# Kernel optimization log

Measured on AMD Instinct MI355X. Metric: run time of the kernel, lower is better.

Reference implementation:

```python
import jax, jax.numpy as jnp
import numpy as np
import math

B, S, D = 16, 2048, 128

def setup_inputs() -> dict:
    key = jax.random.key(0)
    k1, k2, k3, k4 = jax.random.split(key, 4)
    query = jax.random.normal(k1, (B, S, D), dtype=jnp.float32)
    key_t = jax.random.normal(k2, (B, S, D), dtype=jnp.float32)
    value = jax.random.normal(k3, (B, S, D), dtype=jnp.float32)
    attn_mask = jax.random.randint(k4, (B, S, S), 0, 2).astype(bool)
    return {"query": query, "key": key_t, "value": value, "attn_mask": attn_mask}

def reference(query, key, value, attn_mask):
    # score = Q K^T / sqrt(d)  -> [B, Sq, Sk]
    scale = 1.0 / math.sqrt(query.shape[-1])
    score = jnp.einsum('bqd,bkd->bqk', query, key) * scale
    # faithful quirk: masked positions are replaced by the VALUE 1e-9 (not -inf)
    mask_score = jnp.where(attn_mask, jnp.float32(1e-9), score)
    # faithful quirk: softmax over dim=1 (the query axis), as in the torch source
    score_matrix = jax.nn.softmax(mask_score, axis=1)
    # output = softmax(scores) @ V  -> [B, Sq, D]
    output = jnp.einsum('bqk,bkd->bqd', score_matrix, value)
    return output
```

## Files before the change

### kernel.cpp

```cpp
#include <hip/hip_runtime.h>
#include <math.h>

#define NB 16
#define SS 2048
#define DQ 128
#define SCALE 0.08838834764831845f

typedef __bf16 bf16x8 __attribute__((ext_vector_type(8)));
typedef unsigned short ushort8_t __attribute__((ext_vector_type(8)));
typedef float floatx4 __attribute__((ext_vector_type(4)));

__device__ __forceinline__ unsigned short f2bf(float x) {
  unsigned int u = __float_as_uint(x);
  u += 0x7fffu + ((u >> 16) & 1u);
  return (unsigned short)(u >> 16);
}
union FragU { ushort8_t u; bf16x8 b; };
__device__ __forceinline__ bf16x8 ld_frag(const unsigned short* p) {
  FragU t; t.u = *(const ushort8_t*)p; return t.b;
}
__device__ __forceinline__ floatx4 mfma16(bf16x8 a, bf16x8 b, floatx4 c) {
  return __builtin_amdgcn_mfma_f32_16x16x32_bf16(a, b, c, 0, 0, 0);
}

__device__ __forceinline__ void bar_lds() {
  asm volatile("s_waitcnt lgkmcnt(0)\n\ts_barrier" ::: "memory");
}


__global__ void zero_accum(float* __restrict__ O) {
  float* p = O + (size_t)blockIdx.x * SS * DQ + 16 * DQ;
#pragma unroll
  for (int i = 0; i < 8; ++i) p[threadIdx.x + 256 * i] = 0.f;
}

__global__ __launch_bounds__(256, 4) void pass1_colsum(
    const float* __restrict__ Q, const float* __restrict__ K,
    const int* __restrict__ M, float* __restrict__ O)
{
  const int k0  = blockIdx.x * 64;
  const int b   = blockIdx.y;
  const int qc  = blockIdx.z;
  const int tid = threadIdx.x;
  const int w = tid >> 6, lane = tid & 63, l15 = lane & 15, quad = lane >> 4;

  __shared__ unsigned short Kbf[64][136];
  __shared__ unsigned short Qbf[64][136];
  __shared__ float red[4][64];

  const float* Qb = Q + (size_t)b * SS * DQ;
  const float* Kb = K + (size_t)b * SS * DQ;
  const int*   Mb = M + (size_t)b * SS * SS;

  const int srow = tid >> 5;
  const int sc4  = (tid & 31) * 4;

#pragma unroll
  for (int r = 0; r < 8; ++r) {
    int row = srow + r * 8;
    float4 v = *(const float4*)(Kb + (size_t)(k0 + row) * DQ + sc4);
    *(ushort4*)&Kbf[row][sc4] = make_ushort4(f2bf(v.x), f2bf(v.y), f2bf(v.z), f2bf(v.w));
  }

  const int qlane = 16 * w + l15;

  float4 qreg[8];
  int4 mv_nxt[4];
  {
    const int q0 = qc * 512;
#pragma unroll
    for (int r = 0; r < 8; ++r)
      qreg[r] = *(const float4*)(Qb + (size_t)(q0 + srow + r * 8) * DQ + sc4);
#pragma unroll
    for (int i = 0; i < 4; ++i)
      mv_nxt[i] = *(const int4*)(Mb + (size_t)(q0 + qlane) * SS + k0 + 16 * i + quad * 4);
  }

  float colacc[16];
#pragma unroll
  for (int t = 0; t < 16; ++t) colacc[t] = 0.f;

  for (int qi = 0; qi < 8; ++qi) {
    bar_lds();
    int4 mv[4] = {mv_nxt[0], mv_nxt[1], mv_nxt[2], mv_nxt[3]};
#pragma unroll
    for (int r = 0; r < 8; ++r) {
      float4 v = qreg[r];
      *(ushort4*)&Qbf[srow + r * 8][sc4] =
          make_ushort4(f2bf(v.x), f2bf(v.y), f2bf(v.z), f2bf(v.w));
    }
    bar_lds();
    if (qi < 7) {
      const int qn = qc * 512 + (qi + 1) * 64;
#pragma unroll
      for (int r = 0; r < 8; ++r)
        qreg[r] = *(const float4*)(Qb + (size_t)(qn + srow + r * 8) * DQ + sc4);
#pragma unroll
      for (int i = 0; i < 4; ++i)
        mv_nxt[i] = *(const int4*)(Mb + (size_t)(qn + qlane) * SS + k0 + 16 * i + quad * 4);
    }

    floatx4 acc[4];
#pragma unroll
    for (int i = 0; i < 4; ++i) acc[i] = (floatx4){0.f, 0.f, 0.f, 0.f};
#pragma unroll
    for (int d0 = 0; d0 < DQ; d0 += 32) {
      bf16x8 bq = ld_frag(&Qbf[qlane][d0 + quad * 8]);
#pragma unroll
      for (int i = 0; i < 4; ++i) {
        bf16x8 ak = ld_frag(&Kbf[16 * i + l15][d0 + quad * 8]);
        acc[i] = mfma16(ak, bq, acc[i]);
      }
    }
#pragma unroll
    for (int i = 0; i < 4; ++i) {
      int mm[4] = {mv[i].x, mv[i].y, mv[i].z, mv[i].w};
#pragma unroll
      for (int r = 0; r < 4; ++r) {
        float s = mm[r] ? 1e-9f : acc[i][r] * SCALE;
        colacc[i * 4 + r] += __expf(s);
      }
    }
  }

#pragma unroll
  for (int t = 0; t < 16; ++t) {
    colacc[t] += __shfl_xor(colacc[t], 1, 64);
    colacc[t] += __shfl_xor(colacc[t], 2, 64);
    colacc[t] += __shfl_xor(colacc[t], 4, 64);
    colacc[t] += __shfl_xor(colacc[t], 8, 64);
  }
  if (l15 == 0) {
#pragma unroll
    for (int i = 0; i < 4; ++i)
#pragma unroll
      for (int r = 0; r < 4; ++r)
        red[w][16 * i + quad * 4 + r] = colacc[i * 4 + r];
  }
  bar_lds();
  if (tid < 64) {
    float s = red[0][tid] + red[1][tid] + red[2][tid] + red[3][tid];
    atomicAdd(O + (size_t)b * SS * DQ + 16 * DQ + k0 + tid, s);
  }
}

__global__ void combine_linv(float* __restrict__ O) {
  const int b  = blockIdx.x;
  const int jb = blockIdx.y * 4;
  float* Ob = O + (size_t)b * SS * DQ;
#pragma unroll
  for (int it = 0; it < 8; ++it) {
    int k = threadIdx.x + 256 * it;
    float inv = 1.0f / Ob[16 * DQ + k];
#pragma unroll
    for (int j = 0; j < 4; ++j)
      Ob[(size_t)(64 * (jb + j)) * DQ + k] = inv;
  }
}

__global__ __launch_bounds__(256, 2) void pass2_out(
    const float* __restrict__ Q, const float* __restrict__ K,
    const float* __restrict__ V, const int* __restrict__ M,
    float* __restrict__ O)
{
  const int b = blockIdx.y, q0 = blockIdx.x * 64;
  const int tid = threadIdx.x;
  const int w = tid >> 6, lane = tid & 63, l15 = lane & 15, quad = lane >> 4;

  __shared__ unsigned short Kbf[64][136];
  __shared__ unsigned short Es[64][72];
  __shared__ unsigned short Wt[128][72];
  __shared__ float Li[SS];

  const float* Qb = Q + (size_t)b * SS * DQ;
  const float* Kb = K + (size_t)b * SS * DQ;
  const float* Vb = V + (size_t)b * SS * DQ;
  const int*   Mb = M + (size_t)b * SS * SS;

  const int srow = tid >> 5;
  const int sc4  = (tid & 31) * 4;

  {
    const float* src = O + ((size_t)b * SS + q0) * DQ;
#pragma unroll
    for (int r = 0; r < 2; ++r) {
      int idx = (tid + r * 256) * 4;
      *(float4*)&Li[idx] = *(const float4*)(src + idx);
    }
  }
  FragU qf[4];
  {
    const float* qrow = Qb + (size_t)(q0 + 16 * w + l15) * DQ;
#pragma unroll
    for (int i = 0; i < 4; ++i) {
      float4 a = *(const float4*)(qrow + 32 * i + quad * 8);
      float4 c = *(const float4*)(qrow + 32 * i + quad * 8 + 4);
      qf[i].u = (ushort8_t){f2bf(a.x), f2bf(a.y), f2bf(a.z), f2bf(a.w),
                            f2bf(c.x), f2bf(c.y), f2bf(c.z), f2bf(c.w)};
    }
  }

  floatx4 accO[8];
#pragma unroll
  for (int j = 0; j < 8; ++j) accO[j] = (floatx4){0.f, 0.f, 0.f, 0.f};

  const int* mrow = Mb + (size_t)(q0 + 16 * w + l15) * SS;

  float4 kreg[8], vreg[8];
  int4 mv_nxt[4];
  const int vk2 = (tid >> 5) * 2;
  {
#pragma unroll
    for (int r = 0; r < 8; ++r)
      kreg[r] = *(const float4*)(Kb + (size_t)(srow + r * 8) * DQ + sc4);
#pragma unroll
    for (int r = 0; r < 4; ++r) {
      int k2 = vk2 + r * 16;
      vreg[2 * r]     = *(const float4*)(Vb + (size_t)(k2)     * DQ + sc4);
      vreg[2 * r + 1] = *(const float4*)(Vb + (size_t)(k2 + 1) * DQ + sc4);
    }
#pragma unroll
    for (int j = 0; j < 4; ++j)
      mv_nxt[j] = *(const int4*)(mrow + 16 * j + quad * 4);
  }

  for (int k0 = 0; k0 < SS; k0 += 64) {
    bar_lds();
    int4 mv[4] = {mv_nxt[0], mv_nxt[1], mv_nxt[2], mv_nxt[3]};

#pragma unroll
    for (int r = 0; r < 8; ++r) {
      float4 v = kreg[r];
      *(ushort4*)&Kbf[srow + r * 8][sc4] =
          make_ushort4(f2bf(v.x), f2bf(v.y), f2bf(v.z), f2bf(v.w));
    }
#pragma unroll
    for (int r = 0; r < 4; ++r) {
      int k2 = vk2 + r * 16;
      float fa[4] = {vreg[2*r].x, vreg[2*r].y, vreg[2*r].z, vreg[2*r].w};
      float fb[4] = {vreg[2*r+1].x, vreg[2*r+1].y, vreg[2*r+1].z, vreg[2*r+1].w};
#pragma unroll
      for (int i = 0; i < 4; ++i) {
        int d  = sc4 + i;
        int kk = k2 ^ ((((unsigned)d >> 2) & 7) << 3);
        *(ushort2*)&Wt[d][kk] = make_ushort2(f2bf(fa[i]), f2bf(fb[i]));
      }
    }
    bar_lds();

    if (k0 + 64 < SS) {
      const int kn = k0 + 64;
#pragma unroll
      for (int r = 0; r < 8; ++r)
        kreg[r] = *(const float4*)(Kb + (size_t)(kn + srow + r * 8) * DQ + sc4);
#pragma unroll
      for (int r = 0; r < 4; ++r) {
        int k2 = vk2 + r * 16;
        vreg[2 * r]     = *(const float4*)(Vb + (size_t)(kn + k2)     * DQ + sc4);
        vreg[2 * r + 1] = *(const float4*)(Vb + (size_t)(kn + k2 + 1) * DQ + sc4);
      }
#pragma unroll
      for (int j = 0; j < 4; ++j)
        mv_nxt[j] = *(const int4*)(mrow + kn + 16 * j + quad * 4);
    }

    floatx4 acc[4];
#pragma unroll
    for (int j = 0; j < 4; ++j) acc[j] = (floatx4){0.f, 0.f, 0.f, 0.f};
#pragma unroll
    for (int i = 0; i < 4; ++i) {
      bf16x8 bq = qf[i].b;
#pragma unroll
      for (int j = 0; j < 4; ++j) {
        bf16x8 ak = ld_frag(&Kbf[16 * j + l15][32 * i + quad * 8]);
        acc[j] = mfma16(ak, bq, acc[j]);
      }
    }
#pragma unroll
    for (int j = 0; j < 4; ++j) {
      float4 liv = *(const float4*)&Li[k0 + 16 * j + quad * 4];
      float lv[4] = {liv.x, liv.y, liv.z, liv.w};
      int mm[4] = {mv[j].x, mv[j].y, mv[j].z, mv[j].w};
      unsigned short es[4];
#pragma unroll
      for (int r = 0; r < 4; ++r) {
        float s = mm[r] ? 1e-9f : acc[j][r] * SCALE;
        es[r] = f2bf(__expf(s) * lv[r]);
      }
      *(ushort4*)&Es[16 * w + l15][16 * j + quad * 4] =
          make_ushort4(es[0], es[1], es[2], es[3]);
    }
#pragma unroll
    for (int c = 0; c < 2; ++c) {
      bf16x8 be = ld_frag(&Es[16 * w + l15][32 * c + quad * 8]);
#pragma unroll
      for (int j = 0; j < 8; ++j) {
        int d  = 16 * j + l15;
        int kk = (32 * c + quad * 8) ^ ((((unsigned)d >> 2) & 7) << 3);
        bf16x8 aw = ld_frag(&Wt[d][kk]);
        accO[j] = mfma16(aw, be, accO[j]);
      }
    }
  }

#pragma unroll
  for (int j = 0; j < 8; ++j) {
    float* op = O + ((size_t)b * SS + q0 + 16 * w + l15) * DQ + 16 * j + quad * 4;
    *(float4*)op = make_float4(accO[j][0], accO[j][1], accO[j][2], accO[j][3]);
  }
}

extern "C" void kernel_launch(void* const* d_in, const int* in_sizes, int n_in,
                              void* d_out, int out_size, void* d_ws, size_t ws_size,
                              hipStream_t stream) {
  const float* Q = (const float*)d_in[0];
  const float* K = (const float*)d_in[1];
  const float* V = (const float*)d_in[2];
  const int*   M = (const int*)d_in[3];
  float* O = (float*)d_out;
  (void)d_ws; (void)ws_size;

  zero_accum<<<dim3(NB), 256, 0, stream>>>(O);
  pass1_colsum<<<dim3(32, NB, 4), 256, 0, stream>>>(Q, K, M, O);
  combine_linv<<<dim3(NB, 8), 256, 0, stream>>>(O);
  pass2_out<<<dim3(32, NB), 256, 0, stream>>>(Q, K, V, M, O);
}
```

Baseline: 517.8 us.

## Keep pass1 Q/K fragments in registers, halve key tile, use packed bf16 and exp2

Pass1 now loads K and Q fragments straight into MFMA registers instead of staging them through shared memory, which removes the LDS traffic and both barriers per iteration. The key tile drops to 32 columns per block and the grid doubles to keep the GPU filled, with launch bounds relaxed to 3 waves. Both passes switch to hardware packed float2-to-bf16 conversion and exp2 with a folded scale constant, cutting ALU work. Masked scores now give exp2(0)=1 instead of exp(1e-9), a negligible numeric change. The trade-off is that each block re-reads Q for a smaller K slice, so global Q traffic in pass1 doubles.

```diff
diff --git a/kernel.cpp b/kernel.cpp
--- a/kernel.cpp
+++ b/kernel.cpp
@@ -1,21 +1,27 @@
 #include <hip/hip_runtime.h>
+#include <hip/hip_bf16.h>
 #include <math.h>
 
 #define NB 16
 #define SS 2048
 #define DQ 128
 #define SCALE 0.08838834764831845f
+#define EXP2SCALE 0.1275325865719469f
 
 typedef __bf16 bf16x8 __attribute__((ext_vector_type(8)));
 typedef unsigned short ushort8_t __attribute__((ext_vector_type(8)));
 typedef float floatx4 __attribute__((ext_vector_type(4)));
 
-__device__ __forceinline__ unsigned short f2bf(float x) {
-  unsigned int u = __float_as_uint(x);
-  u += 0x7fffu + ((u >> 16) & 1u);
-  return (unsigned short)(u >> 16);
-}
-union FragU { ushort8_t u; bf16x8 b; };
+union FragU { ushort8_t u; bf16x8 b; uint4 i; };
+
+__device__ __forceinline__ unsigned int pk2(float lo, float hi) {
+  union { __hip_bfloat162 h; unsigned int u; } cv;
+  cv.h = __float22bfloat162_rn(make_float2(lo, hi));
+  return cv.u;
+}
+__device__ __forceinline__ uint4 pack8(float4 a, float4 c) {
+  return make_uint4(pk2(a.x, a.y), pk2(a.z, a.w), pk2(c.x, c.y), pk2(c.z, c.w));
+}
 __device__ __forceinline__ bf16x8 ld_frag(const unsigned short* p) {
   FragU t; t.u = *(const ushort8_t*)p; return t.b;
 }
@@ -34,97 +40,97 @@
   for (int i = 0; i < 8; ++i) p[threadIdx.x + 256 * i] = 0.f;
 }
 
-__global__ __launch_bounds__(256, 4) void pass1_colsum(
+__global__ __launch_bounds__(256, 3) void pass1_colsum(
     const float* __restrict__ Q, const float* __restrict__ K,
     const int* __restrict__ M, float* __restrict__ O)
 {
-  const int k0  = blockIdx.x * 64;
+  const int k0  = blockIdx.x * 32;
   const int b   = blockIdx.y;
   const int qc  = blockIdx.z;
   const int tid = threadIdx.x;
   const int w = tid >> 6, lane = tid & 63, l15 = lane & 15, quad = lane >> 4;
 
-  __shared__ unsigned short Kbf[64][136];
-  __shared__ unsigned short Qbf[64][136];
-  __shared__ float red[4][64];
+  __shared__ float red[4][32];
 
   const float* Qb = Q + (size_t)b * SS * DQ;
   const float* Kb = K + (size_t)b * SS * DQ;
   const int*   Mb = M + (size_t)b * SS * SS;
 
-  const int srow = tid >> 5;
-  const int sc4  = (tid & 31) * 4;
-
-#pragma unroll
-  for (int r = 0; r < 8; ++r) {
-    int row = srow + r * 8;
-    float4 v = *(const float4*)(Kb + (size_t)(k0 + row) * DQ + sc4);
-    *(ushort4*)&Kbf[row][sc4] = make_ushort4(f2bf(v.x), f2bf(v.y), f2bf(v.z), f2bf(v.w));
+  FragU kf[2][4];
+#pragma unroll
+  for (int j = 0; j < 2; ++j) {
+    const float* krow = Kb + (size_t)(k0 + 16 * j + l15) * DQ;
+#pragma unroll
+    for (int d0 = 0; d0 < 4; ++d0) {
+      float4 a = *(const float4*)(krow + 32 * d0 + 8 * quad);
+      float4 c = *(const float4*)(krow + 32 * d0 + 8 * quad + 4);
+      kf[j][d0].i = pack8(a, c);
+    }
   }
 
   const int qlane = 16 * w + l15;
+  const int qbase = qc * 512;
 
   float4 qreg[8];
-  int4 mv_nxt[4];
+  int4 mv_nxt[2];
   {
-    const int q0 = qc * 512;
-#pragma unroll
-    for (int r = 0; r < 8; ++r)
-      qreg[r] = *(const float4*)(Qb + (size_t)(q0 + srow + r * 8) * DQ + sc4);
-#pragma unroll
-    for (int i = 0; i < 4; ++i)
-      mv_nxt[i] = *(const int4*)(Mb + (size_t)(q0 + qlane) * SS + k0 + 16 * i + quad * 4);
-  }
-
-  float colacc[16];
-#pragma unroll
-  for (int t = 0; t < 16; ++t) colacc[t] = 0.f;
+    const float* qrow = Qb + (size_t)(qbase + qlane) * DQ;
+#pragma unroll
+    for (int d0 = 0; d0 < 4; ++d0) {
+      qreg[2 * d0]     = *(const float4*)(qrow + 32 * d0 + 8 * quad);
+      qreg[2 * d0 + 1] = *(const float4*)(qrow + 32 * d0 + 8 * quad + 4);
+    }
+    const int* mp = Mb + (size_t)(qbase + qlane) * SS + k0;
+    mv_nxt[0] = *(const int4*)(mp + quad * 4);
+    mv_nxt[1] = *(const int4*)(mp + 16 + quad * 4);
+  }
+
+  float colacc[8];
+#pragma unroll
+  for (int t = 0; t < 8; ++t) colacc[t] = 0.f;
 
   for (int qi = 0; qi < 8; ++qi) {
-    bar_lds();
-    int4 mv[4] = {mv_nxt[0], mv_nxt[1], mv_nxt[2], mv_nxt[3]};
-#pragma unroll
-    for (int r = 0; r < 8; ++r) {
-      float4 v = qreg[r];
-      *(ushort4*)&Qbf[srow + r * 8][sc4] =
-          make_ushort4(f2bf(v.x), f2bf(v.y), f2bf(v.z), f2bf(v.w));
-    }
-    bar_lds();
+    int4 mv[2] = {mv_nxt[0], mv_nxt[1]};
+    FragU qf[4];
+#pragma unroll
+    for (int d0 = 0; d0 < 4; ++d0)
+      qf[d0].i = pack8(qreg[2 * d0], qreg[2 * d0 + 1]);
+
     if (qi < 7) {
-      const int qn = qc * 512 + (qi + 1) * 64;
-#pragma unroll
-      for (int r = 0; r < 8; ++r)
-        qreg[r] = *(const float4*)(Qb + (size_t)(qn + srow + r * 8) * DQ + sc4);
-#pragma unroll
-      for (int i = 0; i < 4; ++i)
-        mv_nxt[i] = *(const int4*)(Mb + (size_t)(qn + qlane) * SS + k0 + 16 * i + quad * 4);
-    }
-
-    floatx4 acc[4];
-#pragma unroll
-    for (int i = 0; i < 4; ++i) acc[i] = (floatx4){0.f, 0.f, 0.f, 0.f};
-#pragma unroll
-    for (int d0 = 0; d0 < DQ; d0 += 32) {
-      bf16x8 bq = ld_frag(&Qbf[qlane][d0 + quad * 8]);
-#pragma unroll
-      for (int i = 0; i < 4; ++i) {
-        bf16x8 ak = ld_frag(&Kbf[16 * i + l15][d0 + quad * 8]);
-        acc[i] = mfma16(ak, bq, acc[i]);
-      }
-    }
-#pragma unroll
-    for (int i = 0; i < 4; ++i) {
-      int mm[4] = {mv[i].x, mv[i].y, mv[i].z, mv[i].w};
+      const int qn = qbase + (qi + 1) * 64 + qlane;
+      const float* qrow = Qb + (size_t)qn * DQ;
+#pragma unroll
+      for (int d0 = 0; d0 < 4; ++d0) {
+        qreg[2 * d0]     = *(const float4*)(qrow + 32 * d0 + 8 * quad);
+        qreg[2 * d0 + 1] = *(const float4*)(qrow + 32 * d0 + 8 * quad + 4);
+      }
+      const int* mp = Mb + (size_t)qn * SS + k0;
+      mv_nxt[0] = *(const int4*)(mp + quad * 4);
+      mv_nxt[1] = *(const int4*)(mp + 16 + quad * 4);
+    }
+
+    floatx4 acc[2];
+    acc[0] = (floatx4){0.f, 0.f, 0.f, 0.f};
+    acc[1] = (floatx4){0.f, 0.f, 0.f, 0.f};
+#pragma unroll
+    for (int d0 = 0; d0 < 4; ++d0) {
+#pragma unroll
+      for (int j = 0; j < 2; ++j)
+        acc[j] = mfma16(kf[j][d0].b, qf[d0].b, acc[j]);
+    }
+#pragma unroll
+    for (int j = 0; j < 2; ++j) {
+      int mm[4] = {mv[j].x, mv[j].y, mv[j].z, mv[j].w};
 #pragma unroll
       for (int r = 0; r < 4; ++r) {
-        float s = mm[r] ? 1e-9f : acc[i][r] * SCALE;
-        colacc[i * 4 + r] += __expf(s);
-      }
-    }
-  }
-
-#pragma unroll
-  for (int t = 0; t < 16; ++t) {
+        float s = mm[r] ? 0.f : acc[j][r] * EXP2SCALE;
+        colacc[j * 4 + r] += exp2f(s);
+      }
+    }
+  }
+
+#pragma unroll
+  for (int t = 0; t < 8; ++t) {
     colacc[t] += __shfl_xor(colacc[t], 1, 64);
     colacc[t] += __shfl_xor(colacc[t], 2, 64);
     colacc[t] += __shfl_xor(colacc[t], 4, 64);
@@ -132,13 +138,13 @@
   }
   if (l15 == 0) {
 #pragma unroll
-    for (int i = 0; i < 4; ++i)
+    for (int j = 0; j < 2; ++j)
 #pragma unroll
       for (int r = 0; r < 4; ++r)
-        red[w][16 * i + quad * 4 + r] = colacc[i * 4 + r];
-  }
-  bar_lds();
-  if (tid < 64) {
+        red[w][16 * j + quad * 4 + r] = colacc[j * 4 + r];
+  }
+  __syncthreads();
+  if (tid < 32) {
     float s = red[0][tid] + red[1][tid] + red[2][tid] + red[3][tid];
     atomicAdd(O + (size_t)b * SS * DQ + 16 * DQ + k0 + tid, s);
   }
@@ -195,8 +201,7 @@
     for (int i = 0; i < 4; ++i) {
       float4 a = *(const float4*)(qrow + 32 * i + quad * 8);
       float4 c = *(const float4*)(qrow + 32 * i + quad * 8 + 4);
-      qf[i].u = (ushort8_t){f2bf(a.x), f2bf(a.y), f2bf(a.z), f2bf(a.w),
-                            f2bf(c.x), f2bf(c.y), f2bf(c.z), f2bf(c.w)};
+      qf[i].i = pack8(a, c);
     }
   }
 
@@ -231,8 +236,7 @@
 #pragma unroll
     for (int r = 0; r < 8; ++r) {
       float4 v = kreg[r];
-      *(ushort4*)&Kbf[srow + r * 8][sc4] =
-          make_ushort4(f2bf(v.x), f2bf(v.y), f2bf(v.z), f2bf(v.w));
+      *(uint2*)&Kbf[srow + r * 8][sc4] = make_uint2(pk2(v.x, v.y), pk2(v.z, v.w));
     }
 #pragma unroll
     for (int r = 0; r < 4; ++r) {
@@ -243,7 +247,7 @@
       for (int i = 0; i < 4; ++i) {
         int d  = sc4 + i;
         int kk = k2 ^ ((((unsigned)d >> 2) & 7) << 3);
-        *(ushort2*)&Wt[d][kk] = make_ushort2(f2bf(fa[i]), f2bf(fb[i]));
+        *(unsigned int*)&Wt[d][kk] = pk2(fa[i], fb[i]);
       }
     }
     bar_lds();
@@ -281,14 +285,14 @@
       float4 liv = *(const float4*)&Li[k0 + 16 * j + quad * 4];
       float lv[4] = {liv.x, liv.y, liv.z, liv.w};
       int mm[4] = {mv[j].x, mv[j].y, mv[j].z, mv[j].w};
-      unsigned short es[4];
+      float ev[4];
 #pragma unroll
       for (int r = 0; r < 4; ++r) {
-        float s = mm[r] ? 1e-9f : acc[j][r] * SCALE;
-        es[r] = f2bf(__expf(s) * lv[r]);
-      }
-      *(ushort4*)&Es[16 * w + l15][16 * j + quad * 4] =
-          make_ushort4(es[0], es[1], es[2], es[3]);
+        float s = mm[r] ? 0.f : acc[j][r] * EXP2SCALE;
+        ev[r] = exp2f(s) * lv[r];
+      }
+      *(uint2*)&Es[16 * w + l15][16 * j + quad * 4] =
+          make_uint2(pk2(ev[0], ev[1]), pk2(ev[2], ev[3]));
     }
 #pragma unroll
     for (int c = 0; c < 2; ++c) {
@@ -321,7 +325,7 @@
   (void)d_ws; (void)ws_size;
 
   zero_accum<<<dim3(NB), 256, 0, stream>>>(O);
-  pass1_colsum<<<dim3(32, NB, 4), 256, 0, stream>>>(Q, K, M, O);
+  pass1_colsum<<<dim3(64, NB, 4), 256, 0, stream>>>(Q, K, M, O);
   combine_linv<<<dim3(NB, 8), 256, 0, stream>>>(O);
   pass2_out<<<dim3(32, NB), 256, 0, stream>>>(Q, K, V, M, O);
 }
```

Result: slower. 635.2 us (+22.7%).
